# Optimization experiments

Hardware: AMD Instinct MI355X
Metric: run time of the kernel (lower is better)

The kernel has to match this reference:

```python
import jax, jax.numpy as jnp
import numpy as np

N_NODES = 10000
N_REL = 200
DIM = 128          # rank * 2
REL_DIM = 128
VIS_DIM = 512
TXT_DIM = 768
N_EDGES = 320000


def _glorot(key, shape):
    fan_in, fan_out = shape[1], shape[0]
    lim = (6.0 / (fan_in + fan_out)) ** 0.5
    return jax.random.uniform(key, shape, jnp.float32, -lim, lim)


def setup_inputs() -> dict:
    key = jax.random.key(0)
    ks = jax.random.split(key, 24)
    inp = {}
    inp['x'] = jax.random.randint(ks[0], (1024, 3), 0, N_NODES)
    inp['edge_index'] = jax.random.randint(ks[1], (2, N_EDGES), 0, N_NODES)
    inp['edge_type'] = jax.random.randint(ks[2], (N_EDGES,), 0, N_REL)
    inp['visual'] = jax.random.normal(ks[3], (N_NODES, VIS_DIM), jnp.float32)
    inp['textual'] = jax.random.normal(ks[4], (N_NODES, TXT_DIM), jnp.float32)
    # embeddings (scaled by 0.001 as in torch init)
    inp['structural_emb'] = jax.random.normal(ks[5], (N_NODES, DIM), jnp.float32) * 0.001
    inp['relation_emb'] = jax.random.normal(ks[6], (N_REL, REL_DIM), jnp.float32) * 0.001
    # three KBGAT convs: w1 [out, 2*in+rel], b1 [out], w2 [1, out]
    cat = 2 * DIM + REL_DIM
    for i, tag in enumerate(['s', 'v', 't']):
        inp[f'W1_{tag}'] = _glorot(ks[7 + 3 * i], (DIM, cat))
        inp[f'b1_{tag}'] = jnp.zeros((DIM,), jnp.float32)
        inp[f'w2_{tag}'] = _glorot(ks[8 + 3 * i], (1, DIM))
    # modality projections
    inp['Wv'] = _glorot(ks[16], (DIM, VIS_DIM))
    inp['bv'] = jnp.zeros((DIM,), jnp.float32)
    inp['Wt'] = _glorot(ks[17], (DIM, TXT_DIM))
    inp['bt'] = jnp.zeros((DIM,), jnp.float32)
    inp['alpha'] = jnp.float32(0.1)
    inp['gamma'] = jnp.float32(0.8)
    return inp


def kbgat_conv(feat, rel_emb, src, dst, edge_type, W1, b1, w2):
    # gather per-edge embeddings: x_i = target, x_j = source (PyG default flow)
    triple = jnp.concatenate([feat[dst], feat[src], rel_emb[edge_type]], axis=1)  # [E, 2*D+R]
    c = triple @ W1.T + b1                                   # [E, D]
    b = jax.nn.leaky_relu(c @ w2[0])                         # [E]
    # segment softmax over destination nodes
    m = jax.ops.segment_max(b, dst, num_segments=N_NODES)
    e = jnp.exp(b - m[dst])
    z = jax.ops.segment_sum(e, dst, num_segments=N_NODES)
    attn = e / z[dst]                                        # [E]
    agg = jax.ops.segment_sum(c * attn[:, None], dst, num_segments=N_NODES)  # [N, D]
    return jax.nn.leaky_relu(agg)


def reference(x, edge_index, edge_type, visual, textual, structural_emb, relation_emb,
              W1_s, b1_s, w2_s, W1_v, b1_v, w2_v, W1_t, b1_t, w2_t,
              Wv, bv, Wt, bt, alpha, gamma):
    src, dst = edge_index[0], edge_index[1]
    h_s = kbgat_conv(structural_emb, relation_emb, src, dst, edge_type, W1_s, b1_s, w2_s)
    vf = visual @ Wv.T + bv
    h_v = kbgat_conv(vf, relation_emb, src, dst, edge_type, W1_v, b1_v, w2_v)
    tf = textual @ Wt.T + bt
    h_t = kbgat_conv(tf, relation_emb, src, dst, edge_type, W1_t, b1_t, w2_t)
    return (1.0 - alpha - gamma) * h_s + alpha * h_v + gamma * h_t
```

## Files before the change

### kernel.cpp

```cpp
#include <hip/hip_runtime.h>
#include <hip/hip_bf16.h>

typedef unsigned short u16;
typedef unsigned int u32;
typedef __bf16 bf16x8 __attribute__((ext_vector_type(8)));
typedef float f32x4 __attribute__((ext_vector_type(4)));

#define DIM 128

__device__ __forceinline__ u16 f2bf_rne(float x) {
  u32 u = __float_as_uint(x);
  return (u16)((u + 0x7fffu + ((u >> 16) & 1u)) >> 16);
}
__device__ __forceinline__ u32 packbf2(float x, float y) {
  return (u32)f2bf_rne(x) | ((u32)f2bf_rne(y) << 16);
}
__device__ __forceinline__ float lrelu(float x) { return x > 0.f ? x : 0.01f * x; }
__device__ __forceinline__ int iclamp(int v, int hi) { return v < 0 ? 0 : (v >= hi ? hi - 1 : v); }
__device__ __forceinline__ float sane(float x) { return (x == x) ? x : 0.f; }

__device__ __forceinline__ float wred_max(float v) {
  #pragma unroll
  for (int o = 32; o > 0; o >>= 1) v = fmaxf(v, __shfl_xor(v, o, 64));
  return v;
}
__device__ __forceinline__ float wred_sum(float v) {
  #pragma unroll
  for (int o = 32; o > 0; o >>= 1) v += __shfl_xor(v, o, 64);
  return v;
}

__global__ void hist_k(const int* __restrict__ dst, int* __restrict__ cnt, int E, int N) {
  int e = blockIdx.x * blockDim.x + threadIdx.x;
  if (e < E) {
    int d = dst[e];
    if (d >= 0 && d < N) atomicAdd(&cnt[d], 1);
  }
}

__global__ __launch_bounds__(1024) void scan_k(const int* __restrict__ cnt,
                                               int* __restrict__ offs, int N) {
  __shared__ int sums[1024];
  int t = threadIdx.x;
  int chunk = (N + 1023) >> 10;
  int base = t * chunk;
  int s = 0;
  for (int i = 0; i < chunk; ++i) { int idx = base + i; if (idx < N) s += cnt[idx]; }
  sums[t] = s;
  __syncthreads();
  for (int off = 1; off < 1024; off <<= 1) {
    int v = (t >= off) ? sums[t - off] : 0;
    __syncthreads();
    sums[t] += v;
    __syncthreads();
  }
  int prefix = (t > 0) ? sums[t - 1] : 0;
  for (int i = 0; i < chunk; ++i) {
    int idx = base + i;
    if (idx < N) { offs[idx] = prefix; prefix += cnt[idx]; }
  }
  if (t == 1023) offs[N] = sums[1023];
}

__global__ void scatter_k(const int* __restrict__ dst, const int* __restrict__ src,
                          const int* __restrict__ etyp,
                          const int* __restrict__ offs,
                          int* __restrict__ cursor, u32* __restrict__ sortedST,
                          int E, int N, int NR) {
  int e = blockIdx.x * blockDim.x + threadIdx.x;
  if (e < E) {
    int d = dst[e];
    if (d >= 0 && d < N) {
      int pos = offs[d] + atomicAdd(&cursor[d], 1);
      if (pos >= 0 && pos < E) {
        u32 s = (u32)iclamp(src[e], N);
        u32 t = (u32)iclamp(etyp[e], NR);
        sortedST[pos] = (t << 16) | s;
      }
    }
  }
}

struct PrepArgs {
  const float* W1[3]; const float* Wmod[3]; int K[3]; int isCopy[3];
  u16* Wc[3];
};
struct PrArgs {
  const float* rel; const float* W1[3]; const float* b1[3];
  const float* bmod[3]; const float* w2[3];
  u16* PrAll; float* qr[3]; int NR;
};
struct GArgs {
  const float* A[3]; const u16* B[3]; const float* w2[3];
  u16* PdAll; u16* PsAll; float* qd[3]; float* qs[3];
  int M; int K[3];
};
struct AgArgs {
  const u32* sortedST; const int* offs;
  const float* qd[3]; const float* qs[3]; const float* qr[3];
  const u16* PdAll; const u16* PsAll; const u16* PrAll;
  const float* alphaP; const float* gammaP;
  float* outp; int N; int NR; int E;
};

__global__ void prep_wc_all(PrepArgs a) {
  int m = blockIdx.z;
  int K = a.K[m];
  int k = blockIdx.x * blockDim.x + threadIdx.x;
  int o = blockIdx.y;
  if (k >= K) return;
  int half = (o >= 128) ? 128 : 0;
  int oo = o & 127;
  const float* W1 = a.W1[m];
  float acc;
  if (a.isCopy[m]) {
    acc = W1[oo * 384 + half + k];
  } else {
    const float* Wm = a.Wmod[m];
    acc = 0.f;
    for (int i = 0; i < 128; ++i)
      acc += W1[oo * 384 + half + i] * Wm[i * K + k];
  }
  a.Wc[m][((size_t)(k >> 5) * 256 + o) * 32 + (k & 31)] = f2bf_rne(acc);
}

__global__ __launch_bounds__(128) void prep_pr_all(PrArgs a) {
  __shared__ float red[128];
  int m = blockIdx.z;
  int r = blockIdx.x;
  if (r >= a.NR) return;
  int o = threadIdx.x;
  const float* W1 = a.W1[m];
  float acc = a.b1[m][o];
  for (int i = 0; i < 128; ++i)
    acc += W1[o * 384 + 256 + i] * a.rel[r * 128 + i];
  const float* bmod = a.bmod[m];
  if (bmod != nullptr) {
    for (int i = 0; i < 128; ++i)
      acc += (W1[o * 384 + i] + W1[o * 384 + 128 + i]) * bmod[i];
  }
  a.PrAll[(size_t)r * 384 + m * 128 + o] = f2bf_rne(acc);
  red[o] = acc * a.w2[m][o];
  __syncthreads();
  for (int s = 64; s > 0; s >>= 1) {
    if (o < s) red[o] += red[o + s];
    __syncthreads();
  }
  if (o == 0) a.qr[m][r] = sane(red[0]);
}

__global__ __launch_bounds__(256) void gemm_fused(GArgs g) {
  __shared__ u16 Als[8 * 64 * 32];
  __shared__ float qpart[4][64];
  int m = blockIdx.y;
  int M = g.M, K = g.K[m];
  int nt = K >> 5;
  const u16* Bpk = g.B[m];
  const float* w2 = g.w2[m];
  int tid = threadIdx.x;
  int lane = tid & 63, wv = tid >> 6;
  int quad = lane >> 4, l16 = lane & 15;
  int row0 = blockIdx.x * 64;

  int srow = tid >> 2;
  int kseg = (tid & 3) * 64;
  int grow = row0 + srow;
  if (grow >= M) grow = M - 1;
  const float* Ag = g.A[m] + (size_t)grow * K;

  const u16* Bpg = Bpk + (size_t)(wv * 64 + l16) * 32 + quad * 8;

  f32x4 acc[4][4];
  #pragma unroll
  for (int rg = 0; rg < 4; ++rg)
    #pragma unroll
    for (int t = 0; t < 4; ++t) acc[rg][t] = (f32x4){0.f, 0.f, 0.f, 0.f};

  int nchunk = (nt + 7) >> 3;
  for (int c = 0; c < nchunk; ++c) {
    int kbase = c << 8;
    __syncthreads();
    #pragma unroll
    for (int i = 0; i < 16; ++i) {
      int kl = kseg + i * 4;
      int kg = kbase + kl;
      if (kg < K) {
        float4 v = *reinterpret_cast<const float4*>(Ag + kg);
        u32* d = reinterpret_cast<u32*>(&Als[((kl >> 5) * 64 + srow) * 32 + (kl & 31)]);
        d[0] = packbf2(v.x, v.y);
        d[1] = packbf2(v.z, v.w);
      }
    }
    __syncthreads();
    int kbR = nt - (c << 3);
    if (kbR > 8) kbR = 8;
    for (int kbl = 0; kbl < kbR; ++kbl) {
      const u16* bp = Bpg + (size_t)((c << 3) + kbl) * 8192;
      bf16x8 b0 = *reinterpret_cast<const bf16x8*>(bp);
      bf16x8 b1 = *reinterpret_cast<const bf16x8*>(bp + 512);
      bf16x8 b2 = *reinterpret_cast<const bf16x8*>(bp + 1024);
      bf16x8 b3 = *reinterpret_cast<const bf16x8*>(bp + 1536);
      #pragma unroll
      for (int rg = 0; rg < 4; ++rg) {
        bf16x8 a = *reinterpret_cast<const bf16x8*>(
            &Als[(kbl * 64 + rg * 16 + l16) * 32 + quad * 8]);
        acc[rg][0] = __builtin_amdgcn_mfma_f32_16x16x32_bf16(a, b0, acc[rg][0], 0, 0, 0);
        acc[rg][1] = __builtin_amdgcn_mfma_f32_16x16x32_bf16(a, b1, acc[rg][1], 0, 0, 0);
        acc[rg][2] = __builtin_amdgcn_mfma_f32_16x16x32_bf16(a, b2, acc[rg][2], 0, 0, 0);
        acc[rg][3] = __builtin_amdgcn_mfma_f32_16x16x32_bf16(a, b3, acc[rg][3], 0, 0, 0);
      }
    }
  }

  u16* PdAll = g.PdAll;
  u16* PsAll = g.PsAll;
  float w2c[4];
  #pragma unroll
  for (int t = 0; t < 4; ++t) w2c[t] = w2[(wv & 1) * 64 + t * 16 + l16];

  #pragma unroll
  for (int rg = 0; rg < 4; ++rg) {
    float part[4];
    #pragma unroll
    for (int r = 0; r < 4; ++r) {
      int rr = row0 + rg * 16 + quad * 4 + r;
      bool ok = rr < M;
      float qp = 0.f;
      #pragma unroll
      for (int t = 0; t < 4; ++t) {
        int cc = (wv & 1) * 64 + t * 16 + l16;
        if (ok) {
          if (wv < 2) PdAll[(size_t)rr * 384 + m * 128 + cc] = f2bf_rne(acc[rg][t][r]);
          else        PsAll[(size_t)rr * 384 + m * 128 + cc] = f2bf_rne(acc[rg][t][r]);
        }
        qp += acc[rg][t][r] * w2c[t];
      }
      #pragma unroll
      for (int mk = 1; mk < 16; mk <<= 1) qp += __shfl_xor(qp, mk, 64);
      part[r] = qp;
    }
    if (l16 == 0) {
      #pragma unroll
      for (int r = 0; r < 4; ++r) qpart[wv][rg * 16 + quad * 4 + r] = part[r];
    }
  }
  __syncthreads();
  if (tid < 128) {
    int row = tid & 63;
    int half = tid >> 6;
    int rr = row0 + row;
    if (rr < M) {
      if (half == 0) g.qd[m][rr] = sane(qpart[0][row] + qpart[1][row]);
      else           g.qs[m][rr] = sane(qpart[2][row] + qpart[3][row]);
    }
  }
}

__global__ __launch_bounds__(256) void aggregate_all(AgArgs a) {
  int n = blockIdx.x * 4 + (threadIdx.x >> 6);
  if (n >= a.N) return;
  int lane = threadIdx.x & 63;
  int E = a.E;
  int eb = a.offs[n], ee = a.offs[n + 1];
  if (eb < 0) eb = 0;
  if (eb > E) eb = E;
  if (ee < eb) ee = eb;
  if (ee > E) ee = E;
  int En = ee - eb;

  float al = a.alphaP[0];
  if (!(al > 0.f && al < 1.f)) al = 0.1f;
  float ga = a.gammaP[0];
  if (!(ga > 0.f && ga < 1.f)) ga = 0.8f;
  float coef[3] = {1.f - al - ga, al, ga};

  float qdn[3];
  #pragma unroll
  for (int m = 0; m < 3; ++m) qdn[m] = sane(a.qd[m][n]);

  const u16* PsAll = a.PsAll;
  const u16* PrAll = a.PrAll;
  int dlo = 2 * lane;

  float rm[3] = {-1e30f, -1e30f, -1e30f};
  float z[3] = {0.f, 0.f, 0.f};
  float a0[3] = {0.f, 0.f, 0.f};
  float a1[3] = {0.f, 0.f, 0.f};
  for (int c0 = 0; c0 < En; c0 += 64) {
    int cn = min(64, En - c0);
    u32 stp = 0;
    float bm[3] = {-1e30f, -1e30f, -1e30f};
    if (lane < cn) {
      stp = a.sortedST[eb + c0 + lane];
      int s = (int)(stp & 0xffffu);
      int t = (int)(stp >> 16);
      #pragma unroll
      for (int m = 0; m < 3; ++m)
        bm[m] = lrelu(qdn[m] + a.qs[m][s] + a.qr[m][t]);
    }
    float wr[3];
    #pragma unroll
    for (int m = 0; m < 3; ++m) {
      float cm = wred_max(bm[m]);
      float nm = fmaxf(rm[m], cm);
      float sc = __expf(fmaxf(rm[m] - nm, -80.f));
      z[m] *= sc; a0[m] *= sc; a1[m] *= sc;
      rm[m] = nm;
      wr[m] = (lane < cn) ? __expf(fmaxf(bm[m] - nm, -80.f)) : 0.f;
      z[m] += wr[m];
    }

    int cnR = (cn + 3) & ~3;
    for (int j = 0; j < cnR; j += 4) {
      u32 stj[4];
      float wj[4][3];
      #pragma unroll
      for (int u = 0; u < 4; ++u) {
        stj[u] = __shfl(stp, j + u, 64);
        wj[u][0] = __shfl(wr[0], j + u, 64);
        wj[u][1] = __shfl(wr[1], j + u, 64);
        wj[u][2] = __shfl(wr[2], j + u, 64);
      }
      u32 pu[4][3], ru[4][3];
      #pragma unroll
      for (int u = 0; u < 4; ++u) {
        const u16* ps = PsAll + (size_t)(stj[u] & 0xffffu) * 384 + dlo;
        const u16* pr = PrAll + (size_t)(stj[u] >> 16) * 384 + dlo;
        #pragma unroll
        for (int m = 0; m < 3; ++m) {
          pu[u][m] = *reinterpret_cast<const u32*>(ps + m * 128);
          ru[u][m] = *reinterpret_cast<const u32*>(pr + m * 128);
        }
      }
      #pragma unroll
      for (int u = 0; u < 4; ++u) {
        #pragma unroll
        for (int m = 0; m < 3; ++m) {
          float ps0 = __uint_as_float(pu[u][m] << 16);
          float ps1 = __uint_as_float(pu[u][m] & 0xffff0000u);
          float pr0 = __uint_as_float(ru[u][m] << 16);
          float pr1 = __uint_as_float(ru[u][m] & 0xffff0000u);
          a0[m] = fmaf(wj[u][m], ps0 + pr0, a0[m]);
          a1[m] = fmaf(wj[u][m], ps1 + pr1, a1[m]);
        }
      }
    }
  }
  #pragma unroll
  for (int m = 0; m < 3; ++m) z[m] = wred_sum(z[m]);

  float o0 = 0.f, o1 = 0.f;
  const u16* pd = a.PdAll + (size_t)n * 384 + dlo;
  #pragma unroll
  for (int m = 0; m < 3; ++m) {
    float h0 = 0.f, h1 = 0.f;
    if (En > 0 && z[m] > 0.f) {
      float rz = 1.f / z[m];
      u32 du = *reinterpret_cast<const u32*>(pd + m * 128);
      float pd0 = __uint_as_float(du << 16), pd1 = __uint_as_float(du & 0xffff0000u);
      h0 = lrelu(pd0 + a0[m] * rz);
      h1 = lrelu(pd1 + a1[m] * rz);
    }
    o0 = fmaf(coef[m], h0, o0);
    o1 = fmaf(coef[m], h1, o1);
  }
  float* op = a.outp + (size_t)n * 128 + dlo;
  op[0] = sane(o0);
  op[1] = sane(o1);
}

extern "C" void kernel_launch(void* const* d_in, const int* in_sizes, int n_in,
                              void* d_out, int out_size, void* d_ws, size_t ws_size,
                              hipStream_t stream) {
  const int* ei        = (const int*)d_in[1];
  const int* et        = (const int*)d_in[2];
  const float* visual  = (const float*)d_in[3];
  const float* textual = (const float*)d_in[4];
  const float* semb    = (const float*)d_in[5];
  const float* relemb  = (const float*)d_in[6];
  const float* W1s = (const float*)d_in[7];
  const float* b1s = (const float*)d_in[8];
  const float* w2s = (const float*)d_in[9];
  const float* W1v = (const float*)d_in[10];
  const float* b1v = (const float*)d_in[11];
  const float* w2v = (const float*)d_in[12];
  const float* W1t = (const float*)d_in[13];
  const float* b1t = (const float*)d_in[14];
  const float* w2t = (const float*)d_in[15];
  const float* Wv  = (const float*)d_in[16];
  const float* bv  = (const float*)d_in[17];
  const float* Wt  = (const float*)d_in[18];
  const float* bt  = (const float*)d_in[19];
  const float* alphaP = (const float*)d_in[20];
  const float* gammaP = (const float*)d_in[21];
  float* outp = (float*)d_out;

  const int E   = in_sizes[2];
  const int N   = in_sizes[5] / DIM;
  const int NR  = in_sizes[6] / DIM;
  const int VIS = in_sizes[3] / N;
  const int TXT = in_sizes[4] / N;
  const int KMAX = (TXT > VIS) ? TXT : VIS;
  int Ks[3] = {DIM, VIS, TXT};
  const int NT64 = (N + 63) / 64;

  const float* W1a[3]   = {W1s, W1v, W1t};
  const float* b1a[3]   = {b1s, b1v, b1t};
  const float* w2a[3]   = {w2s, w2v, w2t};
  const float* Wmoda[3] = {nullptr, Wv, Wt};
  const float* bmoda[3] = {nullptr, bv, bt};
  const float* Amoda[3] = {semb, visual, textual};

  const int* esrc = ei;
  const int* edst = ei + E;
  int egrid = (E + 255) / 256;

  size_t off = 0;
  auto take = [&](size_t bytes) -> size_t {
    size_t o = off;
    off = (off + bytes + 255) & ~(size_t)255;
    return o;
  };
  size_t o_cnt  = take((size_t)2 * N * 4);
  size_t o_offs = take((size_t)(N + 1) * 4);
  size_t o_st   = take((size_t)E * 4);
  size_t meta_end = off;
  size_t o_qdm[3], o_qsm[3], o_qrm[3], o_Wcm[3];
  for (int m = 0; m < 3; ++m) {
    o_qdm[m] = take((size_t)N * 4);
    o_qsm[m] = take((size_t)N * 4);
    o_qrm[m] = take((size_t)NR * 4);
    o_Wcm[m] = take((size_t)256 * Ks[m] * 2);
  }
  size_t o_PrAll = take((size_t)NR * 384 * 2);
  size_t o_PdAll = take((size_t)N * 384 * 2);
  size_t o_PsAll = take((size_t)N * 384 * 2);
  size_t need = off;

  if (ws_size < need) {
    hipMemsetAsync(d_out, 0, (size_t)out_size * 4, stream);
    return;
  }

  char* w = (char*)d_ws;
  int* counts = (int*)(w + o_cnt);
  int* cursor = counts + N;
  int* offs   = (int*)(w + o_offs);
  u32* sortedST = (u32*)(w + o_st);

  hipMemsetAsync(w, 0, meta_end, stream);
  hist_k<<<egrid, 256, 0, stream>>>(edst, counts, E, N);
  scan_k<<<1, 1024, 0, stream>>>(counts, offs, N);
  scatter_k<<<egrid, 256, 0, stream>>>(edst, esrc, et, offs, cursor, sortedST, E, N, NR);

  PrepArgs pa;
  PrArgs ra;
  GArgs ga;
  AgArgs aa;
  ra.rel = relemb; ra.NR = NR;
  ra.PrAll = (u16*)(w + o_PrAll);
  ga.M = N;
  ga.PdAll = (u16*)(w + o_PdAll);
  ga.PsAll = (u16*)(w + o_PsAll);
  for (int m = 0; m < 3; ++m) {
    pa.W1[m] = W1a[m]; pa.Wmod[m] = Wmoda[m]; pa.K[m] = Ks[m];
    pa.isCopy[m] = (m == 0);
    pa.Wc[m] = (u16*)(w + o_Wcm[m]);
    ra.W1[m] = W1a[m]; ra.b1[m] = b1a[m]; ra.bmod[m] = bmoda[m]; ra.w2[m] = w2a[m];
    ra.qr[m] = (float*)(w + o_qrm[m]);
    ga.A[m] = Amoda[m]; ga.B[m] = (const u16*)(w + o_Wcm[m]); ga.w2[m] = w2a[m];
    ga.qd[m] = (float*)(w + o_qdm[m]); ga.qs[m] = (float*)(w + o_qsm[m]);
    ga.K[m] = Ks[m];
    aa.qd[m] = (const float*)(w + o_qdm[m]);
    aa.qs[m] = (const float*)(w + o_qsm[m]);
    aa.qr[m] = (const float*)(w + o_qrm[m]);
  }
  aa.PdAll = (const u16*)(w + o_PdAll);
  aa.PsAll = (const u16*)(w + o_PsAll);
  aa.PrAll = (const u16*)(w + o_PrAll);
  aa.sortedST = sortedST; aa.offs = offs;
  aa.alphaP = alphaP; aa.gammaP = gammaP;
  aa.outp = outp; aa.N = N; aa.NR = NR; aa.E = E;

  prep_wc_all<<<dim3((KMAX + 255) / 256, 256, 3), 256, 0, stream>>>(pa);
  prep_pr_all<<<dim3(NR, 1, 3), 128, 0, stream>>>(ra);
  gemm_fused<<<dim3(NT64, 3), 256, 0, stream>>>(ga);
  aggregate_all<<<(N + 3) / 4, 256, 0, stream>>>(aa);
}
```

Measured before the change: 277.2 us.

## Merge prep kernels and shrink GEMM row tile with padded LDS layout

Folds the two weight-prep kernels into one launch by splitting a flat block index between the Wc builder and the relation projection. This removes one kernel launch and its serialization. The projection GEMM tile drops from 64 to 32 rows per block, which doubles the block count for better occupancy across CUs. The LDS A tile now uses a padded row stride of 40 to reduce bank conflicts, and each thread loads one contiguous 32-wide k segment. The cost is that each B fragment load is reused across half as many rows, so B traffic goes up.

```diff
diff --git a/kernel.cpp b/kernel.cpp
--- a/kernel.cpp
+++ b/kernel.cpp
@@ -7,6 +7,7 @@
 typedef float f32x4 __attribute__((ext_vector_type(4)));
 
 #define DIM 128
+#define LROW 40
 
 __device__ __forceinline__ u16 f2bf_rne(float x) {
   u32 u = __float_as_uint(x);
@@ -82,13 +83,11 @@
 }
 
 struct PrepArgs {
-  const float* W1[3]; const float* Wmod[3]; int K[3]; int isCopy[3];
-  u16* Wc[3];
-};
-struct PrArgs {
-  const float* rel; const float* W1[3]; const float* b1[3];
-  const float* bmod[3]; const float* w2[3];
-  u16* PrAll; float* qr[3]; int NR;
+  const float* W1[3]; const float* Wmod[3]; const float* b1[3];
+  const float* bmod[3]; const float* w2[3]; const float* rel;
+  int K[3]; int isCopy[3];
+  u16* Wc[3]; u16* PrAll; float* qr[3];
+  int NR; int wcBlocks; int xK;
 };
 struct GArgs {
   const float* A[3]; const u16* B[3]; const float* w2[3];
@@ -103,55 +102,63 @@
   float* outp; int N; int NR; int E;
 };
 
-__global__ void prep_wc_all(PrepArgs a) {
-  int m = blockIdx.z;
-  int K = a.K[m];
-  int k = blockIdx.x * blockDim.x + threadIdx.x;
-  int o = blockIdx.y;
-  if (k >= K) return;
-  int half = (o >= 128) ? 128 : 0;
-  int oo = o & 127;
-  const float* W1 = a.W1[m];
-  float acc;
-  if (a.isCopy[m]) {
-    acc = W1[oo * 384 + half + k];
+__global__ __launch_bounds__(256) void prep_all(PrepArgs a) {
+  __shared__ float red[128];
+  int bid = blockIdx.x;
+  int tid = threadIdx.x;
+  if (bid < a.wcBlocks) {
+    int m = bid / (256 * a.xK);
+    int rem = bid % (256 * a.xK);
+    int o = rem / a.xK;
+    int kx = rem % a.xK;
+    int k = kx * 256 + tid;
+    int K = a.K[m];
+    if (k >= K) return;
+    int half = (o >= 128) ? 128 : 0;
+    int oo = o & 127;
+    const float* W1 = a.W1[m];
+    float acc;
+    if (a.isCopy[m]) {
+      acc = W1[oo * 384 + half + k];
+    } else {
+      const float* Wm = a.Wmod[m];
+      acc = 0.f;
+      for (int i = 0; i < 128; ++i)
+        acc += W1[oo * 384 + half + i] * Wm[i * K + k];
+    }
+    a.Wc[m][((size_t)(k >> 5) * 256 + o) * 32 + (k & 31)] = f2bf_rne(acc);
   } else {
-    const float* Wm = a.Wmod[m];
-    acc = 0.f;
-    for (int i = 0; i < 128; ++i)
-      acc += W1[oo * 384 + half + i] * Wm[i * K + k];
-  }
-  a.Wc[m][((size_t)(k >> 5) * 256 + o) * 32 + (k & 31)] = f2bf_rne(acc);
-}
-
-__global__ __launch_bounds__(128) void prep_pr_all(PrArgs a) {
-  __shared__ float red[128];
-  int m = blockIdx.z;
-  int r = blockIdx.x;
-  if (r >= a.NR) return;
-  int o = threadIdx.x;
-  const float* W1 = a.W1[m];
-  float acc = a.b1[m][o];
-  for (int i = 0; i < 128; ++i)
-    acc += W1[o * 384 + 256 + i] * a.rel[r * 128 + i];
-  const float* bmod = a.bmod[m];
-  if (bmod != nullptr) {
-    for (int i = 0; i < 128; ++i)
-      acc += (W1[o * 384 + i] + W1[o * 384 + 128 + i]) * bmod[i];
-  }
-  a.PrAll[(size_t)r * 384 + m * 128 + o] = f2bf_rne(acc);
-  red[o] = acc * a.w2[m][o];
-  __syncthreads();
-  for (int s = 64; s > 0; s >>= 1) {
-    if (o < s) red[o] += red[o + s];
+    int p = bid - a.wcBlocks;
+    int m = p / a.NR;
+    int r = p % a.NR;
+    int o = tid;
+    bool act = (o < 128);
+    float acc = 0.f;
+    if (act) {
+      const float* W1 = a.W1[m];
+      acc = a.b1[m][o];
+      for (int i = 0; i < 128; ++i)
+        acc += W1[o * 384 + 256 + i] * a.rel[r * 128 + i];
+      const float* bmod = a.bmod[m];
+      if (bmod != nullptr) {
+        for (int i = 0; i < 128; ++i)
+          acc += (W1[o * 384 + i] + W1[o * 384 + 128 + i]) * bmod[i];
+      }
+      a.PrAll[(size_t)r * 384 + m * 128 + o] = f2bf_rne(acc);
+      red[o] = acc * a.w2[m][o];
+    }
     __syncthreads();
-  }
-  if (o == 0) a.qr[m][r] = sane(red[0]);
+    for (int s = 64; s > 0; s >>= 1) {
+      if (o < s) red[o] += red[o + s];
+      __syncthreads();
+    }
+    if (o == 0) a.qr[m][r] = sane(red[0]);
+  }
 }
 
 __global__ __launch_bounds__(256) void gemm_fused(GArgs g) {
-  __shared__ u16 Als[8 * 64 * 32];
-  __shared__ float qpart[4][64];
+  __shared__ u16 Als[8 * 32 * LROW];
+  __shared__ float qpart[4][32];
   int m = blockIdx.y;
   int M = g.M, K = g.K[m];
   int nt = K >> 5;
@@ -160,19 +167,20 @@
   int tid = threadIdx.x;
   int lane = tid & 63, wv = tid >> 6;
   int quad = lane >> 4, l16 = lane & 15;
-  int row0 = blockIdx.x * 64;
-
-  int srow = tid >> 2;
-  int kseg = (tid & 3) * 64;
+  int row0 = blockIdx.x * 32;
+
+  int srow = tid >> 3;
+  int skb  = tid & 7;
   int grow = row0 + srow;
   if (grow >= M) grow = M - 1;
-  const float* Ag = g.A[m] + (size_t)grow * K;
+  const float* Ag = g.A[m] + (size_t)grow * K + skb * 32;
+  u32* wbase = reinterpret_cast<u32*>(&Als[(skb * 32 + srow) * LROW]);
 
   const u16* Bpg = Bpk + (size_t)(wv * 64 + l16) * 32 + quad * 8;
 
-  f32x4 acc[4][4];
-  #pragma unroll
-  for (int rg = 0; rg < 4; ++rg)
+  f32x4 acc[2][4];
+  #pragma unroll
+  for (int rg = 0; rg < 2; ++rg)
     #pragma unroll
     for (int t = 0; t < 4; ++t) acc[rg][t] = (f32x4){0.f, 0.f, 0.f, 0.f};
 
@@ -180,15 +188,15 @@
   for (int c = 0; c < nchunk; ++c) {
     int kbase = c << 8;
     __syncthreads();
-    #pragma unroll
-    for (int i = 0; i < 16; ++i) {
-      int kl = kseg + i * 4;
-      int kg = kbase + kl;
-      if (kg < K) {
-        float4 v = *reinterpret_cast<const float4*>(Ag + kg);
-        u32* d = reinterpret_cast<u32*>(&Als[((kl >> 5) * 64 + srow) * 32 + (kl & 31)]);
-        d[0] = packbf2(v.x, v.y);
-        d[1] = packbf2(v.z, v.w);
+    {
+      int kg0 = kbase + skb * 32;
+      if (kg0 < K) {
+        #pragma unroll
+        for (int i = 0; i < 8; ++i) {
+          float4 v = *reinterpret_cast<const float4*>(Ag + kbase + i * 4);
+          wbase[i * 2]     = packbf2(v.x, v.y);
+          wbase[i * 2 + 1] = packbf2(v.z, v.w);
+        }
       }
     }
     __syncthreads();
@@ -201,9 +209,9 @@
       bf16x8 b2 = *reinterpret_cast<const bf16x8*>(bp + 1024);
       bf16x8 b3 = *reinterpret_cast<const bf16x8*>(bp + 1536);
       #pragma unroll
-      for (int rg = 0; rg < 4; ++rg) {
+      for (int rg = 0; rg < 2; ++rg) {
         bf16x8 a = *reinterpret_cast<const bf16x8*>(
-            &Als[(kbl * 64 + rg * 16 + l16) * 32 + quad * 8]);
+            &Als[(kbl * 32 + rg * 16 + l16) * LROW + quad * 8]);
         acc[rg][0] = __builtin_amdgcn_mfma_f32_16x16x32_bf16(a, b0, acc[rg][0], 0, 0, 0);
         acc[rg][1] = __builtin_amdgcn_mfma_f32_16x16x32_bf16(a, b1, acc[rg][1], 0, 0, 0);
         acc[rg][2] = __builtin_amdgcn_mfma_f32_16x16x32_bf16(a, b2, acc[rg][2], 0, 0, 0);
@@ -219,7 +227,7 @@
   for (int t = 0; t < 4; ++t) w2c[t] = w2[(wv & 1) * 64 + t * 16 + l16];
 
   #pragma unroll
-  for (int rg = 0; rg < 4; ++rg) {
+  for (int rg = 0; rg < 2; ++rg) {
     float part[4];
     #pragma unroll
     for (int r = 0; r < 4; ++r) {
@@ -245,9 +253,9 @@
     }
   }
   __syncthreads();
-  if (tid < 128) {
-    int row = tid & 63;
-    int half = tid >> 6;
+  if (tid < 64) {
+    int row = tid & 31;
+    int half = tid >> 5;
     int rr = row0 + row;
     if (rr < M) {
       if (half == 0) g.qd[m][rr] = sane(qpart[0][row] + qpart[1][row]);
@@ -402,7 +410,7 @@
   const int TXT = in_sizes[4] / N;
   const int KMAX = (TXT > VIS) ? TXT : VIS;
   int Ks[3] = {DIM, VIS, TXT};
-  const int NT64 = (N + 63) / 64;
+  const int NT32 = (N + 31) / 32;
 
   const float* W1a[3]   = {W1s, W1v, W1t};
   const float* b1a[3]   = {b1s, b1v, b1t};
@@ -454,20 +462,22 @@
   scatter_k<<<egrid, 256, 0, stream>>>(edst, esrc, et, offs, cursor, sortedST, E, N, NR);
 
   PrepArgs pa;
-  PrArgs ra;
   GArgs ga;
   AgArgs aa;
-  ra.rel = relemb; ra.NR = NR;
-  ra.PrAll = (u16*)(w + o_PrAll);
+  pa.rel = relemb; pa.NR = NR;
+  pa.xK = (KMAX + 255) / 256;
+  pa.wcBlocks = 3 * 256 * pa.xK;
+  pa.PrAll = (u16*)(w + o_PrAll);
   ga.M = N;
   ga.PdAll = (u16*)(w + o_PdAll);
   ga.PsAll = (u16*)(w + o_PsAll);
   for (int m = 0; m < 3; ++m) {
-    pa.W1[m] = W1a[m]; pa.Wmod[m] = Wmoda[m]; pa.K[m] = Ks[m];
+    pa.W1[m] = W1a[m]; pa.Wmod[m] = Wmoda[m]; pa.b1[m] = b1a[m];
+    pa.bmod[m] = bmoda[m]; pa.w2[m] = w2a[m];
+    pa.K[m] = Ks[m];
     pa.isCopy[m] = (m == 0);
     pa.Wc[m] = (u16*)(w + o_Wcm[m]);
-    ra.W1[m] = W1a[m]; ra.b1[m] = b1a[m]; ra.bmod[m] = bmoda[m]; ra.w2[m] = w2a[m];
-    ra.qr[m] = (float*)(w + o_qrm[m]);
+    pa.qr[m] = (float*)(w + o_qrm[m]);
     ga.A[m] = Amoda[m]; ga.B[m] = (const u16*)(w + o_Wcm[m]); ga.w2[m] = w2a[m];
     ga.qd[m] = (float*)(w + o_qdm[m]); ga.qs[m] = (float*)(w + o_qsm[m]);
     ga.K[m] = Ks[m];
@@ -482,8 +492,7 @@
   aa.alphaP = alphaP; aa.gammaP = gammaP;
   aa.outp = outp; aa.N = N; aa.NR = NR; aa.E = E;
 
-  prep_wc_all<<<dim3((KMAX + 255) / 256, 256, 3), 256, 0, stream>>>(pa);
-  prep_pr_all<<<dim3(NR, 1, 3), 128, 0, stream>>>(ra);
-  gemm_fused<<<dim3(NT64, 3), 256, 0, stream>>>(ga);
+  prep_all<<<pa.wcBlocks + 3 * NR, 256, 0, stream>>>(pa);
+  gemm_fused<<<dim3(NT32, 3), 256, 0, stream>>>(ga);
   aggregate_all<<<(N + 3) / 4, 256, 0, stream>>>(aa);
 }
```

Result: no change. 279.1 us (+0.7%).
